# Optimization experiments

Measured on AMD Instinct MI355X. Metric: run time of the kernel, lower is better.

## Reference

```python
import jax, jax.numpy as jnp
import numpy as np


def quat_to_rot(q):
    # q: [B, 4] = (x, y, z, w); same math as from_quaternion in the source.
    x, y, z, w = q[:, 0], q[:, 1], q[:, 2], q[:, 3]
    tx, ty, tz = 2.0 * x, 2.0 * y, 2.0 * z
    twx, twy, twz = tx * w, ty * w, tz * w
    txx, txy, txz = tx * x, ty * x, tz * x
    tyy, tyz, tzz = ty * y, tz * y, tz * z
    r = jnp.stack([1.0 - (tyy + tzz), txy - twz, txz + twy,
                   txy + twz, 1.0 - (txx + tzz), tyz - twx,
                   txz - twy, tyz + twx, 1.0 - (txx + tyy)], axis=-1)
    return r.reshape(-1, 3, 3)


def matrix_from_params(transfos):
    B, N = transfos.shape
    R = quat_to_rot(transfos[:, :4])
    if N == 10:
        S = jax.vmap(jnp.diag)(transfos[:, -3:])
    else:
        S = jnp.broadcast_to(jnp.eye(3, dtype=transfos.dtype), (B, 3, 3))
    SR = jnp.matmul(S, R)
    if N == 7:
        t = transfos[:, 4:7][..., None]
    else:
        t = jnp.zeros((B, 3, 1), transfos.dtype)
    return jnp.concatenate([SR, t], axis=2)  # [B, 3, 4]


def spatial_transformer_3d(img, transfos, min_ref_grid, max_ref_grid):
    B, H, W, D, C = img.shape  # ref_size_xyz = (W, H, D) per the source
    theta = matrix_from_params(transfos)  # [B, 3, 4]

    xs = jnp.linspace(min_ref_grid[0], max_ref_grid[0], W)
    ys = jnp.linspace(min_ref_grid[1], max_ref_grid[1], H)
    zs = jnp.linspace(min_ref_grid[2], max_ref_grid[2], D)
    mz, my, mx = jnp.meshgrid(zs, ys, xs, indexing='ij')  # (D, H, W), x fastest
    Nel = D * H * W
    grid = jnp.stack([mx.ravel(), my.ravel(), mz.ravel(),
                      jnp.ones(Nel, dtype=img.dtype)], axis=0)  # (4, Nel)
    pts = jnp.einsum('bij,jn->bin', theta, grid)  # (B, 3, Nel)

    Wf, Hf, Df = float(W), float(H), float(D)
    cx = (Wf - 1.0) / (max_ref_grid[0] - min_ref_grid[0])
    cy = (Hf - 1.0) / (max_ref_grid[1] - min_ref_grid[1])
    cz = (Df - 1.0) / (max_ref_grid[2] - min_ref_grid[2])
    ix = cx * pts[:, 0, :] - cx * min_ref_grid[0]
    iy = cy * pts[:, 1, :] - cy * min_ref_grid[1]
    iz = cz * pts[:, 2, :] - cz * min_ref_grid[2]

    # padding_mode in {'zeros','min'}: validity mask for out-of-grid points
    valid = ((ix >= 0.0) & (ix <= Wf - 1.0) &
             (iy >= 0.0) & (iy <= Hf - 1.0) &
             (iz >= 0.0) & (iz <= Df - 1.0)).astype(img.dtype)[..., None]  # (B, Nel, 1)

    ix0 = jnp.clip(jnp.floor(ix), 0.0, Wf - 1.0)
    iy0 = jnp.clip(jnp.floor(iy), 0.0, Hf - 1.0)
    iz0 = jnp.clip(jnp.floor(iz), 0.0, Df - 1.0)

    imf = img.reshape(B, H * W * D, C)
    acc = jnp.zeros((B, Nel, C), img.dtype)
    for ox in (0.0, 1.0):
        for oy in (0.0, 1.0):
            for oz in (0.0, 1.0):
                gx, gy, gz = ix0 + ox, iy0 + oy, iz0 + oz  # corner coords
                w = (jnp.clip(1.0 - jnp.abs(ix - gx), 0.0, 1.0) *
                     jnp.clip(1.0 - jnp.abs(iy - gy), 0.0, 1.0) *
                     jnp.clip(1.0 - jnp.abs(iz - gz), 0.0, 1.0))
                gxi = jnp.clip(gx, 0.0, Wf - 1.0).astype(jnp.int32)
                gyi = jnp.clip(gy, 0.0, Hf - 1.0).astype(jnp.int32)
                gzi = jnp.clip(gz, 0.0, Df - 1.0).astype(jnp.int32)
                lin = (gyi * W + gxi) * D + gzi  # row-major index into [H, W, D]
                v = jnp.take_along_axis(imf, lin[..., None], axis=1)  # (B, Nel, C)
                acc = acc + w[..., None] * v

    # padding_mode == 'min': fill out-of-grid voxels with the per-volume minimum
    fill = jnp.min(img, axis=(1, 2, 3, 4))[:, None, None]  # (B, 1, 1)
    out = valid * acc + (1.0 - valid) * fill
    # grid was flattened in (z, y, x) order with x fastest -> back to (H, W, D)
    out = out.reshape(B, D, H, W, C).transpose(0, 2, 3, 1, 4)
    return out


def setup_inputs() -> dict:
    key = jax.random.key(0)
    k1, k2 = jax.random.split(key)
    img = jax.random.normal(k1, (4, 160, 160, 160, 1), dtype=jnp.float32)
    transfos = jax.random.normal(k2, (4, 7), dtype=jnp.float32)
    return {"img": img, "transfos": transfos}


def reference(img, transfos):
    min_ref_grid = (-1.0, -1.0, -1.0)
    max_ref_grid = (1.0, 1.0, 1.0)
    return spatial_transformer_3d(img, transfos, min_ref_grid, max_ref_grid)
```

## Files before the change

kernel.cpp:

```cpp
#include <hip/hip_runtime.h>

#define HH 160
#define WW 160
#define DD 160
#define BB 4

__device__ __forceinline__ unsigned mapf(float f) {
    unsigned b = __float_as_uint(f);
    return (b & 0x80000000u) ? ~b : (b | 0x80000000u);
}
__device__ __forceinline__ float unmapf(unsigned k) {
    unsigned b = (k & 0x80000000u) ? (k ^ 0x80000000u) : ~k;
    return __uint_as_float(b);
}

__global__ void setup_kernel(const float* __restrict__ transfos,
                             unsigned* __restrict__ minkey,
                             double* __restrict__ cst) {
    int b = threadIdx.x;
    if (b >= BB) return;
    minkey[b] = 0xFFFFFFFFu;
    const float* q = transfos + b * 7;
    double x = q[0], y = q[1], z = q[2], w = q[3];
    double tx = 2.0 * x, ty = 2.0 * y, tz = 2.0 * z;
    double twx = tx * w, twy = ty * w, twz = tz * w;
    double txx = tx * x, txy = ty * x, txz = tz * x;
    double tyy = ty * y, tyz = tz * y, tzz = tz * z;
    double R[3][3] = {
        {1.0 - (tyy + tzz), txy - twz,         txz + twy},
        {txy + twz,         1.0 - (txx + tzz), tyz - twx},
        {txz - twy,         tyz + twx,         1.0 - (txx + tyy)}
    };
    double t[3] = {(double)q[4], (double)q[5], (double)q[6]};
    for (int r = 0; r < 3; r++) {
        double c0 = 79.5 * (t[r] - R[r][0] - R[r][1] - R[r][2] + 1.0);
        cst[b * 12 + r * 4 + 0] = R[r][0];
        cst[b * 12 + r * 4 + 1] = R[r][1];
        cst[b * 12 + r * 4 + 2] = R[r][2];
        cst[b * 12 + r * 4 + 3] = c0;
    }
}

__global__ __launch_bounds__(256) void min_kernel(const float4* __restrict__ img4,
                                                  unsigned* __restrict__ minkey) {
    const int b = blockIdx.y;
    const int NB = HH * WW * DD / 4;
    float m = 3.4e38f;
    for (int i = blockIdx.x * blockDim.x + threadIdx.x; i < NB;
         i += gridDim.x * blockDim.x) {
        float4 v = img4[(size_t)b * NB + i];
        m = fminf(m, fminf(fminf(v.x, v.y), fminf(v.z, v.w)));
    }
    #pragma unroll
    for (int o = 32; o >= 1; o >>= 1) m = fminf(m, __shfl_down(m, o));
    __shared__ float s[4];
    int lane = threadIdx.x & 63, wid = threadIdx.x >> 6;
    if (lane == 0) s[wid] = m;
    __syncthreads();
    if (threadIdx.x == 0) {
        m = fminf(fminf(s[0], s[1]), fminf(s[2], s[3]));
        atomicMin(&minkey[b], mapf(m));
    }
}

__global__ __launch_bounds__(256) void st3d_kernel(const float* __restrict__ img,
                                                   const double* __restrict__ cst,
                                                   const unsigned* __restrict__ minkey,
                                                   float* __restrict__ out) {
    const int b = blockIdx.z;
    const int y = blockIdx.y;
    const int i = blockIdx.x * 256 + threadIdx.x;
    const int x = i / 160;
    const int z = i - 160 * x;

    const double* c = cst + b * 12;
    const double dx = (double)x, dy = (double)y, dz = (double)z;
    const double ixd = fma(c[0], dx, fma(c[1], dy, fma(c[2], dz, c[3])));
    const double iyd = fma(c[4], dx, fma(c[5], dy, fma(c[6], dz, c[7])));
    const double izd = fma(c[8], dx, fma(c[9], dy, fma(c[10], dz, c[11])));

    const float fill = unmapf(minkey[b]);
    float res = fill;
    const bool valid = (ixd >= 0.0) && (ixd <= 159.0) && (iyd >= 0.0) &&
                       (iyd <= 159.0) && (izd >= 0.0) && (izd <= 159.0);
    if (valid) {
        double flx = floor(ixd), fly = floor(iyd), flz = floor(izd);
        int x0 = (int)flx, y0 = (int)fly, z0 = (int)flz;
        float fx = (float)(ixd - flx), fy = (float)(iyd - fly), fz = (float)(izd - flz);
        int x1 = min(x0 + 1, 159), y1 = min(y0 + 1, 159), z1 = min(z0 + 1, 159);
        const float* base = img + (size_t)b * (HH * WW * DD);
        const float* p00 = base + ((size_t)y0 * WW + x0) * DD;
        const float* p01 = base + ((size_t)y0 * WW + x1) * DD;
        const float* p10 = base + ((size_t)y1 * WW + x0) * DD;
        const float* p11 = base + ((size_t)y1 * WW + x1) * DD;
        float v000 = p00[z0], v001 = p00[z1];
        float v010 = p10[z0], v011 = p10[z1];
        float v100 = p01[z0], v101 = p01[z1];
        float v110 = p11[z0], v111 = p11[z1];
        float wx0 = 1.0f - fx, wx1 = fx;
        float wy0 = 1.0f - fy, wy1 = fy;
        float wz0 = 1.0f - fz, wz1 = fz;
        float acc;
        acc  = ((wx0 * wy0) * wz0) * v000;
        acc += ((wx0 * wy0) * wz1) * v001;
        acc += ((wx0 * wy1) * wz0) * v010;
        acc += ((wx0 * wy1) * wz1) * v011;
        acc += ((wx1 * wy0) * wz0) * v100;
        acc += ((wx1 * wy0) * wz1) * v101;
        acc += ((wx1 * wy1) * wz0) * v110;
        acc += ((wx1 * wy1) * wz1) * v111;
        res = acc;
    }
    out[(size_t)(b * HH + y) * (WW * DD) + i] = res;
}

extern "C" void kernel_launch(void* const* d_in, const int* in_sizes, int n_in,
                              void* d_out, int out_size, void* d_ws, size_t ws_size,
                              hipStream_t stream) {
    const float* img = (const float*)d_in[0];
    const float* transfos = (const float*)d_in[1];
    float* out = (float*)d_out;
    unsigned* minkey = (unsigned*)d_ws;
    double* cst = (double*)((char*)d_ws + 64);

    setup_kernel<<<1, 64, 0, stream>>>(transfos, minkey, cst);
    min_kernel<<<dim3(256, BB), 256, 0, stream>>>((const float4*)img, minkey);
    st3d_kernel<<<dim3(100, 160, BB), 256, 0, stream>>>(img, cst, minkey, out);
}
```

Measured before the change: 140.7 us.

## Fuse setup into min kernel, vectorize sampler to four outputs per thread

Merges the transform-setup kernel into the min-reduction kernel and swaps the minkey initialization for a memset. The min kernel now does a fixed four float4 loads per thread over a wider grid instead of a grid-stride loop. The sampler computes four consecutive z outputs per thread, stepping coordinates incrementally, and writes them with one non-temporal vector store. Launch overhead and store instruction count should drop, at the cost of less parallelism per sample in the gather kernel.

```diff
diff --git a/kernel.cpp b/kernel.cpp
--- a/kernel.cpp
+++ b/kernel.cpp
@@ -4,6 +4,8 @@
 #define WW 160
 #define DD 160
 #define BB 4
+
+typedef float vfloat4 __attribute__((ext_vector_type(4)));
 
 __device__ __forceinline__ unsigned mapf(float f) {
     unsigned b = __float_as_uint(f);
@@ -14,52 +16,58 @@
     return __uint_as_float(b);
 }
 
-__global__ void setup_kernel(const float* __restrict__ transfos,
-                             unsigned* __restrict__ minkey,
-                             double* __restrict__ cst) {
-    int b = threadIdx.x;
-    if (b >= BB) return;
-    minkey[b] = 0xFFFFFFFFu;
-    const float* q = transfos + b * 7;
-    double x = q[0], y = q[1], z = q[2], w = q[3];
-    double tx = 2.0 * x, ty = 2.0 * y, tz = 2.0 * z;
-    double twx = tx * w, twy = ty * w, twz = tz * w;
-    double txx = tx * x, txy = ty * x, txz = tz * x;
-    double tyy = ty * y, tyz = tz * y, tzz = tz * z;
-    double R[3][3] = {
-        {1.0 - (tyy + tzz), txy - twz,         txz + twy},
-        {txy + twz,         1.0 - (txx + tzz), tyz - twx},
-        {txz - twy,         tyz + twx,         1.0 - (txx + tyy)}
-    };
-    double t[3] = {(double)q[4], (double)q[5], (double)q[6]};
-    for (int r = 0; r < 3; r++) {
-        double c0 = 79.5 * (t[r] - R[r][0] - R[r][1] - R[r][2] + 1.0);
-        cst[b * 12 + r * 4 + 0] = R[r][0];
-        cst[b * 12 + r * 4 + 1] = R[r][1];
-        cst[b * 12 + r * 4 + 2] = R[r][2];
-        cst[b * 12 + r * 4 + 3] = c0;
-    }
-}
-
-__global__ __launch_bounds__(256) void min_kernel(const float4* __restrict__ img4,
-                                                  unsigned* __restrict__ minkey) {
+__global__ __launch_bounds__(256) void min_cst_kernel(const float4* __restrict__ img4,
+                                                      const float* __restrict__ transfos,
+                                                      unsigned* __restrict__ minkey,
+                                                      double* __restrict__ cst) {
     const int b = blockIdx.y;
     const int NB = HH * WW * DD / 4;
-    float m = 3.4e38f;
-    for (int i = blockIdx.x * blockDim.x + threadIdx.x; i < NB;
-         i += gridDim.x * blockDim.x) {
-        float4 v = img4[(size_t)b * NB + i];
-        m = fminf(m, fminf(fminf(v.x, v.y), fminf(v.z, v.w)));
-    }
+    const size_t base = (size_t)b * NB;
+    const int idx = blockIdx.x * 256 + threadIdx.x;
+    const int S = 262144;
+
+    float4 v0 = img4[base + idx];
+    float4 v1 = img4[base + idx + S];
+    float4 v2 = img4[base + idx + 2 * S];
+    float4 v3 = make_float4(3.4e38f, 3.4e38f, 3.4e38f, 3.4e38f);
+    if (idx + 3 * S < NB) v3 = img4[base + idx + 3 * S];
+
+    float m = fminf(fminf(fminf(v0.x, v0.y), fminf(v0.z, v0.w)),
+                    fminf(fminf(v1.x, v1.y), fminf(v1.z, v1.w)));
+    m = fminf(m, fminf(fminf(v2.x, v2.y), fminf(v2.z, v2.w)));
+    m = fminf(m, fminf(fminf(v3.x, v3.y), fminf(v3.z, v3.w)));
+
     #pragma unroll
     for (int o = 32; o >= 1; o >>= 1) m = fminf(m, __shfl_down(m, o));
     __shared__ float s[4];
-    int lane = threadIdx.x & 63, wid = threadIdx.x >> 6;
+    const int lane = threadIdx.x & 63, wid = threadIdx.x >> 6;
     if (lane == 0) s[wid] = m;
     __syncthreads();
     if (threadIdx.x == 0) {
         m = fminf(fminf(s[0], s[1]), fminf(s[2], s[3]));
         atomicMin(&minkey[b], mapf(m));
+    }
+
+    if (blockIdx.x == 0 && blockIdx.y == 0 && threadIdx.x < BB) {
+        const int bb = threadIdx.x;
+        const float* q = transfos + bb * 7;
+        double x = q[0], y = q[1], z = q[2], w = q[3];
+        double tx = 2.0 * x, ty = 2.0 * y, tz = 2.0 * z;
+        double twx = tx * w, twy = ty * w, twz = tz * w;
+        double txx = tx * x, txy = ty * x, txz = tz * x;
+        double tyy = ty * y, tyz = tz * y, tzz = tz * z;
+        double R[3][3] = {
+            {1.0 - (tyy + tzz), txy - twz,         txz + twy},
+            {txy + twz,         1.0 - (txx + tzz), tyz - twx},
+            {txz - twy,         tyz + twx,         1.0 - (txx + tyy)}
+        };
+        double t[3] = {(double)q[4], (double)q[5], (double)q[6]};
+        for (int r = 0; r < 3; r++) {
+            cst[bb * 12 + r * 4 + 0] = R[r][0];
+            cst[bb * 12 + r * 4 + 1] = R[r][1];
+            cst[bb * 12 + r * 4 + 2] = R[r][2];
+            cst[bb * 12 + r * 4 + 3] = 79.5 * (t[r] - R[r][0] - R[r][1] - R[r][2] + 1.0);
+        }
     }
 }
 
@@ -69,49 +77,59 @@
                                                    float* __restrict__ out) {
     const int b = blockIdx.z;
     const int y = blockIdx.y;
-    const int i = blockIdx.x * 256 + threadIdx.x;
-    const int x = i / 160;
-    const int z = i - 160 * x;
+    const int t = blockIdx.x * 256 + threadIdx.x;
+    const int x = t / 40;
+    const int zq = (t - 40 * x) * 4;
 
     const double* c = cst + b * 12;
-    const double dx = (double)x, dy = (double)y, dz = (double)z;
-    const double ixd = fma(c[0], dx, fma(c[1], dy, fma(c[2], dz, c[3])));
-    const double iyd = fma(c[4], dx, fma(c[5], dy, fma(c[6], dz, c[7])));
-    const double izd = fma(c[8], dx, fma(c[9], dy, fma(c[10], dz, c[11])));
+    const double c2 = c[2], c6 = c[6], c10 = c[10];
+    const double dx = (double)x, dy = (double)y, dz = (double)zq;
+    double ixd = fma(c[0], dx, fma(c[1], dy, fma(c2, dz, c[3])));
+    double iyd = fma(c[4], dx, fma(c[5], dy, fma(c6, dz, c[7])));
+    double izd = fma(c[8], dx, fma(c[9], dy, fma(c10, dz, c[11])));
 
     const float fill = unmapf(minkey[b]);
-    float res = fill;
-    const bool valid = (ixd >= 0.0) && (ixd <= 159.0) && (iyd >= 0.0) &&
-                       (iyd <= 159.0) && (izd >= 0.0) && (izd <= 159.0);
-    if (valid) {
-        double flx = floor(ixd), fly = floor(iyd), flz = floor(izd);
-        int x0 = (int)flx, y0 = (int)fly, z0 = (int)flz;
-        float fx = (float)(ixd - flx), fy = (float)(iyd - fly), fz = (float)(izd - flz);
-        int x1 = min(x0 + 1, 159), y1 = min(y0 + 1, 159), z1 = min(z0 + 1, 159);
-        const float* base = img + (size_t)b * (HH * WW * DD);
-        const float* p00 = base + ((size_t)y0 * WW + x0) * DD;
-        const float* p01 = base + ((size_t)y0 * WW + x1) * DD;
-        const float* p10 = base + ((size_t)y1 * WW + x0) * DD;
-        const float* p11 = base + ((size_t)y1 * WW + x1) * DD;
-        float v000 = p00[z0], v001 = p00[z1];
-        float v010 = p10[z0], v011 = p10[z1];
-        float v100 = p01[z0], v101 = p01[z1];
-        float v110 = p11[z0], v111 = p11[z1];
-        float wx0 = 1.0f - fx, wx1 = fx;
-        float wy0 = 1.0f - fy, wy1 = fy;
-        float wz0 = 1.0f - fz, wz1 = fz;
-        float acc;
-        acc  = ((wx0 * wy0) * wz0) * v000;
-        acc += ((wx0 * wy0) * wz1) * v001;
-        acc += ((wx0 * wy1) * wz0) * v010;
-        acc += ((wx0 * wy1) * wz1) * v011;
-        acc += ((wx1 * wy0) * wz0) * v100;
-        acc += ((wx1 * wy0) * wz1) * v101;
-        acc += ((wx1 * wy1) * wz0) * v110;
-        acc += ((wx1 * wy1) * wz1) * v111;
-        res = acc;
+    const float* base = img + (size_t)b * (HH * WW * DD);
+
+    vfloat4 r;
+    #pragma unroll
+    for (int k = 0; k < 4; k++) {
+        float res = fill;
+        const bool valid = (ixd >= 0.0) && (ixd <= 159.0) && (iyd >= 0.0) &&
+                           (iyd <= 159.0) && (izd >= 0.0) && (izd <= 159.0);
+        if (valid) {
+            double flx = floor(ixd), fly = floor(iyd), flz = floor(izd);
+            int x0 = (int)flx, y0 = (int)fly, z0 = (int)flz;
+            float fx = (float)(ixd - flx), fy = (float)(iyd - fly), fz = (float)(izd - flz);
+            int x1 = min(x0 + 1, 159), y1 = min(y0 + 1, 159), z1 = min(z0 + 1, 159);
+            const float* p00 = base + ((size_t)y0 * WW + x0) * DD;
+            const float* p01 = base + ((size_t)y0 * WW + x1) * DD;
+            const float* p10 = base + ((size_t)y1 * WW + x0) * DD;
+            const float* p11 = base + ((size_t)y1 * WW + x1) * DD;
+            float v000 = p00[z0], v001 = p00[z1];
+            float v010 = p10[z0], v011 = p10[z1];
+            float v100 = p01[z0], v101 = p01[z1];
+            float v110 = p11[z0], v111 = p11[z1];
+            float wx0 = 1.0f - fx, wx1 = fx;
+            float wy0 = 1.0f - fy, wy1 = fy;
+            float wz0 = 1.0f - fz, wz1 = fz;
+            float acc;
+            acc  = ((wx0 * wy0) * wz0) * v000;
+            acc += ((wx0 * wy0) * wz1) * v001;
+            acc += ((wx0 * wy1) * wz0) * v010;
+            acc += ((wx0 * wy1) * wz1) * v011;
+            acc += ((wx1 * wy0) * wz0) * v100;
+            acc += ((wx1 * wy0) * wz1) * v101;
+            acc += ((wx1 * wy1) * wz0) * v110;
+            acc += ((wx1 * wy1) * wz1) * v111;
+            res = acc;
+        }
+        r[k] = res;
+        ixd += c2; iyd += c6; izd += c10;
     }
-    out[(size_t)(b * HH + y) * (WW * DD) + i] = res;
+
+    vfloat4* outp = (vfloat4*)(out + (size_t)(b * HH + y) * (WW * DD) + x * DD + zq);
+    __builtin_nontemporal_store(r, outp);
 }
 
 extern "C" void kernel_launch(void* const* d_in, const int* in_sizes, int n_in,
@@ -123,7 +141,7 @@
     unsigned* minkey = (unsigned*)d_ws;
     double* cst = (double*)((char*)d_ws + 64);
 
-    setup_kernel<<<1, 64, 0, stream>>>(transfos, minkey, cst);
-    min_kernel<<<dim3(256, BB), 256, 0, stream>>>((const float4*)img, minkey);
-    st3d_kernel<<<dim3(100, 160, BB), 256, 0, stream>>>(img, cst, minkey, out);
+    (void)hipMemsetAsync(minkey, 0xFF, BB * sizeof(unsigned), stream);
+    min_cst_kernel<<<dim3(1024, BB), 256, 0, stream>>>((const float4*)img, transfos, minkey, cst);
+    st3d_kernel<<<dim3(25, 160, BB), 256, 0, stream>>>(img, cst, minkey, out);
 }
```

Result: slower. 175.2 us (+24.6%).
